# Optimization experiments

Hardware: AMD Instinct MI355X
Metric: run time of the kernel (lower is better)

The kernel has to match this reference:

```python
import jax, jax.numpy as jnp
import numpy as np

D_MODEL = 1024


def setup_inputs() -> dict:
    key = jax.random.key(0)
    ks = jax.random.split(key, 9)
    d = D_MODEL
    s = 1.0 / np.sqrt(d)
    return {
        "x": jax.random.normal(ks[0], (4, 2048, d), dtype=jnp.float32),
        "w_q": jax.random.normal(ks[1], (d, d), dtype=jnp.float32) * s,
        "b_q": jnp.zeros((d,), dtype=jnp.float32),
        "w_k": jax.random.normal(ks[2], (d, d), dtype=jnp.float32) * s,
        "b_k": jnp.zeros((d,), dtype=jnp.float32),
        "w_v": jax.random.normal(ks[3], (d, d), dtype=jnp.float32) * s,
        "b_v": jnp.zeros((d,), dtype=jnp.float32),
        "w_out": jax.random.normal(ks[4], (d, d), dtype=jnp.float32) * s,
        "b_out": jnp.zeros((d,), dtype=jnp.float32),
    }


def reference(x, w_q, b_q, w_k, b_k, w_v, b_v, w_out, b_out):
    d_model = x.shape[-1]
    # torch Linear: y = x @ W^T + b
    Q = jnp.einsum("bsd,ed->bse", x, w_q) + b_q
    K = jnp.einsum("bsd,ed->bse", x, w_k) + b_k
    V = jnp.einsum("bsd,ed->bse", x, w_v) + b_v
    scores = jnp.einsum("bqd,bkd->bqk", Q, K) / jnp.sqrt(jnp.float32(d_model)).astype(x.dtype)
    attn = jax.nn.softmax(scores, axis=-1)
    out = jnp.einsum("bqk,bkd->bqd", attn, V)
    return jnp.einsum("bsd,ed->bse", out, w_out) + b_out
```

## Files before the change

kernel.cpp:

```cpp
#include <hip/hip_runtime.h>


typedef __bf16 bf16x8 __attribute__((ext_vector_type(8)));
typedef float f32x4 __attribute__((ext_vector_type(4)));

__device__ __forceinline__ unsigned short f32_to_bf16(float f) {
  unsigned int u = __float_as_uint(f);
  u += 0x7fffu + ((u >> 16) & 1u);
  return (unsigned short)(u >> 16);
}

__device__ __forceinline__ ushort4 cvt4(float4 f) {
  ushort4 u;
  u.x = f32_to_bf16(f.x);
  u.y = f32_to_bf16(f.y);
  u.z = f32_to_bf16(f.z);
  u.w = f32_to_bf16(f.w);
  return u;
}

__device__ __forceinline__ void load_lds16(const void* g, void* l) {
  __builtin_amdgcn_global_load_lds(
      (const __attribute__((address_space(1))) void*)g,
      (__attribute__((address_space(3))) void*)l, 16, 0, 0);
}

__global__ __launch_bounds__(256) void prep(
    const float4* __restrict__ x, const float4* __restrict__ wq,
    const float4* __restrict__ wk, const float4* __restrict__ wv,
    const float4* __restrict__ wo, const float4* __restrict__ bq,
    const float4* __restrict__ bk, ushort4* __restrict__ xb,
    ushort4* __restrict__ wqk, ushort4* __restrict__ wvb,
    ushort4* __restrict__ wob, float4* __restrict__ bqk) {
  const int NX = 2097152;
  const int NW = 262144;
  int i = blockIdx.x * 256 + threadIdx.x;
  if (i < NX) {
    xb[i] = cvt4(x[i]);
  } else if (i < NX + NW) {
    int j = i - NX;
    wqk[j] = cvt4(wq[j]);
  } else if (i < NX + 2 * NW) {
    int j = i - NX - NW;
    wqk[NW + j] = cvt4(wk[j]);
  } else if (i < NX + 3 * NW) {
    int j = i - NX - 2 * NW;
    wvb[j] = cvt4(wv[j]);
  } else if (i < NX + 4 * NW) {
    int j = i - NX - 3 * NW;
    wob[j] = cvt4(wo[j]);
  } else if (i < NX + 4 * NW + 512) {
    int j = i - NX - 4 * NW;
    bqk[j] = (j < 256) ? bq[j] : bk[j - 256];
  }
}

__global__ __launch_bounds__(512, 2) void gemm_bt256dp(
    const unsigned short* __restrict__ A, const unsigned short* __restrict__ B,
    void* __restrict__ C, const float* __restrict__ bias,
    int M, int N, int K, float alpha, int out_bf16, int lda, int ldb,
    long long sA, long long sB, long long sC) {
  __shared__ unsigned short As[3][2][128 * 64];
  __shared__ unsigned short Bs[2][2][128 * 64];

  const int hw = blockIdx.x + gridDim.x * (blockIdx.y + gridDim.y * blockIdx.z);
  const int nwg = gridDim.x * gridDim.y * gridDim.z;
  const int lg = (hw & 7) * (nwg >> 3) + (hw >> 3);
  const int bn = lg % gridDim.x;
  const int rem = lg / gridDim.x;
  const int bm = rem % gridDim.y;
  const int bz = rem / gridDim.y;

  A += (long long)bz * sA;
  B += (long long)bz * sB;

  const int tid = threadIdx.x;
  const int lane = tid & 63, wave = tid >> 6;
  const int wr = wave >> 2;
  const int wc = wave & 3;
  const int l16 = lane & 15, quad = lane >> 4;
  const int wbh = wc >> 1;
  const int wbr = (wc & 1) * 64 + l16;
  const int pc0 = (quad ^ (l16 & 7)) * 8;
  const int pc1 = ((4 + quad) ^ (l16 & 7)) * 8;

  const int srow = tid >> 3;
  const int lch = (tid & 7) ^ (srow & 7);
  const unsigned short* gA0 = A + (long long)(bm * 256 + srow) * lda + lch * 8;
  const unsigned short* gB0 = B + (long long)(bn * 256 + srow) * ldb + lch * 8;

  f32x4 acc[8][4] = {};
  bf16x8 af[2][2];
  bf16x8 bf[4][2];

  const int NT = K >> 6;

#define STA(BUF, H, KT)                                                     \
  do {                                                                      \
    const unsigned short* _s =                                              \
        gA0 + (long long)(H) * 128 * lda + (long long)(KT) * 64;            \
    char* _d = (char*)&As[BUF][H][0] + wave * 1024;                         \
    load_lds16(_s, _d);                                                     \
    load_lds16(_s + (long long)64 * lda, _d + 8192);                        \
  } while (0)
#define STB(BUF, H, KT)                                                     \
  do {                                                                      \
    const unsigned short* _s =                                              \
        gB0 + (long long)(H) * 128 * ldb + (long long)(KT) * 64;            \
    char* _d = (char*)&Bs[BUF][H][0] + wave * 1024;                         \
    load_lds16(_s, _d);                                                     \
    load_lds16(_s + (long long)64 * ldb, _d + 8192);                        \
  } while (0)

#define DSAq(BUF, MIP)                                                      \
  do {                                                                      \
    _Pragma("unroll") for (int m2 = 0; m2 < 2; ++m2) {                      \
      const unsigned short* _r =                                            \
          &As[BUF][wr][(((MIP) * 2 + m2) * 16 + l16) * 64];                 \
      af[m2][0] = *(const bf16x8*)(_r + pc0);                               \
      af[m2][1] = *(const bf16x8*)(_r + pc1);                               \
    }                                                                       \
  } while (0)

#define DSBq(BUF)                                                           \
  do {                                                                      \
    _Pragma("unroll") for (int ni = 0; ni < 4; ++ni) {                      \
      const unsigned short* _r = &Bs[BUF][wbh][(wbr + ni * 16) * 64];       \
      bf[ni][0] = *(const bf16x8*)(_r + pc0);                               \
      bf[ni][1] = *(const bf16x8*)(_r + pc1);                               \
    }                                                                       \
  } while (0)

#define MMq(MIP)                                                            \
  do {                                                                      \
    _Pragma("unroll") for (int m2 = 0; m2 < 2; ++m2)                        \
        _Pragma("unroll") for (int ni = 0; ni < 4; ++ni) {                  \
      f32x4* _a = &acc[(MIP) * 2 + m2][ni];                                 \
      *_a = __builtin_amdgcn_mfma_f32_16x16x32_bf16(af[m2][0], bf[ni][0],   \
                                                    *_a, 0, 0, 0);          \
      *_a = __builtin_amdgcn_mfma_f32_16x16x32_bf16(af[m2][1], bf[ni][1],   \
                                                    *_a, 0, 0, 0);          \
    }                                                                       \
  } while (0)

#define BARx() __builtin_amdgcn_s_barrier()
#define WLGx() asm volatile("s_waitcnt lgkmcnt(0)" ::: "memory")
#define WVM8() asm volatile("s_waitcnt vmcnt(8)" ::: "memory")
#define PR1() __builtin_amdgcn_s_setprio(1)
#define PR0() __builtin_amdgcn_s_setprio(0)

  STA(0, 0, 0);
  STA(0, 1, 0);
  STB(0, 0, 0);
  STB(0, 1, 0);
  STA(1, 0, 1);
  STA(1, 1, 1);
  STB(1, 0, 1);
  STB(1, 1, 1);
  WVM8();
  BARx();

  int a = 0;
  for (int t = 0; t < NT; ++t) {
    const int b = t & 1;
    int a2 = a + 2;
    if (a2 >= 3) a2 -= 3;
    const int kt2 = (t + 2 < NT) ? t + 2 : NT - 1;
    DSBq(b);
    DSAq(a, 0);
    STA(a2, 0, kt2);
    BARx();
    WLGx();
    PR1();
    MMq(0);
    PR0();
    BARx();
    DSAq(a, 1);
    STA(a2, 1, kt2);
    BARx();
    WLGx();
    PR1();
    MMq(1);
    PR0();
    BARx();
    DSAq(a, 2);
    STB(b, 0, kt2);
    BARx();
    WLGx();
    PR1();
    MMq(2);
    PR0();
    BARx();
    DSAq(a, 3);
    STB(b, 1, kt2);
    BARx();
    WLGx();
    PR1();
    MMq(3);
    PR0();
    WVM8();
    BARx();
    ++a;
    if (a == 3) a = 0;
  }
  asm volatile("s_waitcnt vmcnt(0)" ::: "memory");

  const long long orow0 = (long long)bm * 256 + wr * 128 + quad * 4;
  const int ocol0 = bn * 256 + wc * 64 + l16;
  if (out_bf16) {
    unsigned short* Cp = (unsigned short*)C + (long long)bz * sC;
#pragma unroll
    for (int mi = 0; mi < 8; ++mi)
#pragma unroll
      for (int ni = 0; ni < 4; ++ni) {
        const int col = ocol0 + ni * 16;
        const float bv = bias ? bias[col] : 0.f;
#pragma unroll
        for (int r = 0; r < 4; ++r) {
          const float o = acc[mi][ni][r] * alpha + bv;
          Cp[(orow0 + mi * 16 + r) * N + col] = f32_to_bf16(o);
        }
      }
  } else {
    float* Cp = (float*)C + (long long)bz * sC;
#pragma unroll
    for (int mi = 0; mi < 8; ++mi)
#pragma unroll
      for (int ni = 0; ni < 4; ++ni) {
        const int col = ocol0 + ni * 16;
        const float bv = bias ? bias[col] : 0.f;
#pragma unroll
        for (int r = 0; r < 4; ++r) {
          const float o = acc[mi][ni][r] * alpha + bv;
          Cp[(orow0 + mi * 16 + r) * N + col] = o;
        }
      }
  }
#undef STA
#undef STB
#undef DSAq
#undef DSBq
#undef MMq
#undef BARx
#undef WLGx
#undef WVM8
#undef PR1
#undef PR0
}

__global__ __launch_bounds__(512, 2) void gemm_bt128x256(
    const unsigned short* __restrict__ A, const unsigned short* __restrict__ B,
    void* __restrict__ C, const float* __restrict__ bias,
    int M, int N, int K, float alpha, int out_bf16, int bias_row,
    int lda, int ldb, long long sA, long long sB, long long sC) {
  __shared__ unsigned short As[3][128][64];
  __shared__ unsigned short Bs[3][256][64];

  const int hw = blockIdx.x + gridDim.x * (blockIdx.y + gridDim.y * blockIdx.z);
  const int nwg = gridDim.x * gridDim.y * gridDim.z;
  const int lg = (hw & 7) * (nwg >> 3) + (hw >> 3);
  const int bn = lg % gridDim.x;
  const int rem = lg / gridDim.x;
  const int bm = rem % gridDim.y;
  const int bz = rem / gridDim.y;

  A += (long long)bz * sA;
  B += (long long)bz * sB;

  const int tid = threadIdx.x;
  const int lane = tid & 63, wave = tid >> 6;
  const int wr = wave >> 2;
  const int wc = wave & 3;
  const int l16 = lane & 15, quad = lane >> 4;
  const int pc0 = (quad ^ (l16 & 7)) * 8;
  const int pc1 = ((4 + quad) ^ (l16 & 7)) * 8;

  const int srow = tid >> 3;
  const int lch = (tid & 7) ^ (srow & 7);
  const unsigned short* gA0 = A + (long long)(bm * 128 + srow) * lda + lch * 8;
  const unsigned short* gB0 = B + (long long)(bn * 256 + srow) * ldb + lch * 8;

  f32x4 acc[4][4] = {};
  bf16x8 af[2][2];
  bf16x8 bf[4][2];

  const int NT = K >> 6;

#define STG_A(BUF, KT)                                                      \
  do {                                                                      \
    const unsigned short* _s = gA0 + (long long)(KT) * 64;                  \
    char* _d = (char*)&As[BUF][0][0] + wave * 1024;                         \
    load_lds16(_s, _d);                                                     \
    load_lds16(_s + (long long)64 * lda, _d + 8192);                        \
  } while (0)
#define STG_B(BUF, KT, J0, JN)                                              \
  do {                                                                      \
    const unsigned short* _s = gB0 + (long long)(KT) * 64;                  \
    char* _d = (char*)&Bs[BUF][0][0] + wave * 1024;                         \
    _Pragma("unroll") for (int _j = (J0); _j < (JN); ++_j)                  \
        load_lds16(_s + (long long)(_j * 64) * ldb, _d + _j * 8192);        \
  } while (0)

#define DSA(BUF, P)                                                         \
  do {                                                                      \
    _Pragma("unroll") for (int m2 = 0; m2 < 2; ++m2) {                      \
      const unsigned short* _r =                                            \
          &As[BUF][wr * 64 + ((P) * 2 + m2) * 16 + l16][0];                 \
      af[m2][0] = *(const bf16x8*)(_r + pc0);                               \
      af[m2][1] = *(const bf16x8*)(_r + pc1);                               \
    }                                                                       \
  } while (0)

#define DSB(BUF)                                                            \
  do {                                                                      \
    _Pragma("unroll") for (int ni = 0; ni < 4; ++ni) {                      \
      const unsigned short* _r = &Bs[BUF][wc * 64 + ni * 16 + l16][0];      \
      bf[ni][0] = *(const bf16x8*)(_r + pc0);                               \
      bf[ni][1] = *(const bf16x8*)(_r + pc1);                               \
    }                                                                       \
  } while (0)

#define MM(P)                                                               \
  do {                                                                      \
    _Pragma("unroll") for (int m2 = 0; m2 < 2; ++m2)                        \
        _Pragma("unroll") for (int ni = 0; ni < 4; ++ni) {                  \
      f32x4* _a = &acc[(P) * 2 + m2][ni];                                   \
      *_a = __builtin_amdgcn_mfma_f32_16x16x32_bf16(af[m2][0], bf[ni][0],   \
                                                    *_a, 0, 0, 0);          \
      *_a = __builtin_amdgcn_mfma_f32_16x16x32_bf16(af[m2][1], bf[ni][1],   \
                                                    *_a, 0, 0, 0);          \
    }                                                                       \
  } while (0)

#define BAR() __builtin_amdgcn_s_barrier()
#define WLG() asm volatile("s_waitcnt lgkmcnt(0)" ::: "memory")
#define WVM6() asm volatile("s_waitcnt vmcnt(6)" ::: "memory")
#define P1x() __builtin_amdgcn_s_setprio(1)
#define P0x() __builtin_amdgcn_s_setprio(0)

  STG_A(0, 0);
  STG_B(0, 0, 0, 4);
  STG_A(1, 1);
  STG_B(1, 1, 0, 4);
  WVM6();
  BAR();

  int cur = 0;
  for (int t = 0; t < NT; ++t) {
    int b2 = cur + 2;
    if (b2 >= 3) b2 -= 3;
    const int kt = (t + 2 < NT) ? t + 2 : NT - 1;
    DSB(cur);
    DSA(cur, 0);
    STG_A(b2, kt);
    STG_B(b2, kt, 0, 1);
    BAR();
    WLG();
    P1x();
    MM(0);
    P0x();
    BAR();
    DSA(cur, 1);
    STG_B(b2, kt, 1, 4);
    BAR();
    WLG();
    P1x();
    MM(1);
    P0x();
    WVM6();
    BAR();
    ++cur;
    if (cur == 3) cur = 0;
  }
  asm volatile("s_waitcnt vmcnt(0)" ::: "memory");

  const long long orow0 = (long long)bm * 128 + wr * 64 + quad * 4;
  const int ocol0 = bn * 256 + wc * 64 + l16;
  if (out_bf16) {
    unsigned short* Cp = (unsigned short*)C + (long long)bz * sC;
#pragma unroll
    for (int mi = 0; mi < 4; ++mi)
#pragma unroll
      for (int ni = 0; ni < 4; ++ni) {
        const int col = ocol0 + ni * 16;
        const float bcol = (bias && !bias_row) ? bias[col] : 0.f;
#pragma unroll
        for (int r = 0; r < 4; ++r) {
          const float bv =
              (bias && bias_row) ? bias[orow0 + mi * 16 + r] : bcol;
          const float o = acc[mi][ni][r] * alpha + bv;
          Cp[(orow0 + mi * 16 + r) * N + col] = f32_to_bf16(o);
        }
      }
  } else {
    float* Cp = (float*)C + (long long)bz * sC;
#pragma unroll
    for (int mi = 0; mi < 4; ++mi)
#pragma unroll
      for (int ni = 0; ni < 4; ++ni) {
        const int col = ocol0 + ni * 16;
        const float bcol = (bias && !bias_row) ? bias[col] : 0.f;
#pragma unroll
        for (int r = 0; r < 4; ++r) {
          const float bv =
              (bias && bias_row) ? bias[orow0 + mi * 16 + r] : bcol;
          const float o = acc[mi][ni][r] * alpha + bv;
          Cp[(orow0 + mi * 16 + r) * N + col] = o;
        }
      }
  }
#undef STG_A
#undef STG_B
#undef DSA
#undef DSB
#undef MM
#undef BAR
#undef WLG
#undef WVM6
#undef P1x
#undef P0x
}

__global__ __launch_bounds__(256) void softmax_rows(
    const float* __restrict__ S, unsigned short* __restrict__ P) {
  const long long row = blockIdx.x;
  const float* s = S + row * 2048;
  const int t = threadIdx.x;
  float v[8];
  float mx = -3.4e38f;
#pragma unroll
  for (int i = 0; i < 8; i++) {
    v[i] = s[t + i * 256];
    mx = fmaxf(mx, v[i]);
  }
#pragma unroll
  for (int o = 32; o >= 1; o >>= 1) mx = fmaxf(mx, __shfl_xor(mx, o));
  __shared__ float red[4], red2[4];
  if ((t & 63) == 0) red[t >> 6] = mx;
  __syncthreads();
  mx = fmaxf(fmaxf(red[0], red[1]), fmaxf(red[2], red[3]));
  float sum = 0.f;
#pragma unroll
  for (int i = 0; i < 8; i++) {
    v[i] = __expf(v[i] - mx);
    sum += v[i];
  }
#pragma unroll
  for (int o = 32; o >= 1; o >>= 1) sum += __shfl_xor(sum, o);
  if ((t & 63) == 0) red2[t >> 6] = sum;
  __syncthreads();
  sum = red2[0] + red2[1] + red2[2] + red2[3];
  const float inv = 1.0f / sum;
  unsigned short* p = P + row * 2048;
#pragma unroll
  for (int i = 0; i < 8; i++) p[t + i * 256] = f32_to_bf16(v[i] * inv);
}

extern "C" void kernel_launch(void* const* d_in, const int* in_sizes, int n_in,
                              void* d_out, int out_size, void* d_ws,
                              size_t ws_size, hipStream_t stream) {
  const float* x = (const float*)d_in[0];
  const float* wq = (const float*)d_in[1];
  const float* bq = (const float*)d_in[2];
  const float* wk = (const float*)d_in[3];
  const float* bk = (const float*)d_in[4];
  const float* wv = (const float*)d_in[5];
  const float* bv = (const float*)d_in[6];
  const float* wo = (const float*)d_in[7];
  const float* bo = (const float*)d_in[8];
  float* out = (float*)d_out;
  char* ws = (char*)d_ws;
  const size_t MB = 1ull << 20;

  unsigned short* xb  = (unsigned short*)(ws + 0);
  unsigned short* wqk = (unsigned short*)(ws + 16 * MB);
  unsigned short* wvb = (unsigned short*)(ws + 20 * MB);
  unsigned short* wob = (unsigned short*)(ws + 22 * MB);
  unsigned short* QKm = (unsigned short*)(ws + 24 * MB);
  unsigned short* VT  = (unsigned short*)(ws + 56 * MB);
  float*          S   = (float*)(ws + 72 * MB);
  float*          bqk = (float*)(ws + 72 * MB);
  unsigned short* P   = QKm;
  unsigned short* O   = xb;

  prep<<<dim3(12290), dim3(256), 0, stream>>>(
      (const float4*)x, (const float4*)wq, (const float4*)wk,
      (const float4*)wv, (const float4*)wo, (const float4*)bq,
      (const float4*)bk, (ushort4*)xb, (ushort4*)wqk, (ushort4*)wvb,
      (ushort4*)wob, (float4*)bqk);

  gemm_bt256dp<<<dim3(8, 32, 1), dim3(512), 0, stream>>>(
      xb, wqk, QKm, bqk, 8192, 2048, 1024, 1.f, 1, 1024, 1024, 0, 0, 0);

  gemm_bt128x256<<<dim3(32, 8, 1), dim3(512), 0, stream>>>(
      wvb, xb, VT, bv, 1024, 8192, 1024, 1.f, 1, 1, 1024, 1024, 0, 0, 0);

  gemm_bt256dp<<<dim3(8, 8, 4), dim3(512), 0, stream>>>(
      QKm, QKm + 1024, S, nullptr, 2048, 2048, 1024, 0.03125f, 0, 2048, 2048,
      2048ll * 2048, 2048ll * 2048, 2048ll * 2048);

  softmax_rows<<<dim3(8192), dim3(256), 0, stream>>>(S, P);

  gemm_bt128x256<<<dim3(4, 16, 4), dim3(512), 0, stream>>>(
      P, VT, O, nullptr, 2048, 1024, 2048, 1.f, 1, 0, 2048, 8192,
      2048ll * 2048, 2048ll, 2048ll * 1024);

  gemm_bt128x256<<<dim3(4, 64, 1), dim3(512), 0, stream>>>(
      O, wob, out, bo, 8192, 1024, 1024, 1.f, 0, 0, 1024, 1024, 0, 0, 0);
}
```

Before: 297.5 us.

## Fuse all attention stages into one persistent kernel with grid barriers

Replaces the six separate launches (prep, QK proj, V proj, scores, softmax, PV, out proj) with one persistent 256-block kernel. Stages are separated by a software grid barrier built on an atomic counter, and shared memory is carved manually per phase. This removes per-launch overhead and inter-kernel gaps. In exchange it pins occupancy at one block per CU, makes the V-projection run serially after the QK tile in the same block, and depends on all 256 blocks being co-resident to avoid deadlock.

```diff
diff --git a/kernel.cpp b/kernel.cpp
--- a/kernel.cpp
+++ b/kernel.cpp
@@ -3,11 +3,14 @@
 
 typedef __bf16 bf16x8 __attribute__((ext_vector_type(8)));
 typedef float f32x4 __attribute__((ext_vector_type(4)));
-
-__device__ __forceinline__ unsigned short f32_to_bf16(float f) {
+typedef unsigned short ush;
+
+__device__ unsigned int g_bar_cnt;
+
+__device__ __forceinline__ ush f32_to_bf16(float f) {
   unsigned int u = __float_as_uint(f);
   u += 0x7fffu + ((u >> 16) & 1u);
-  return (unsigned short)(u >> 16);
+  return (ush)(u >> 16);
 }
 
 __device__ __forceinline__ ushort4 cvt4(float4 f) {
@@ -25,54 +28,27 @@
       (__attribute__((address_space(3))) void*)l, 16, 0, 0);
 }
 
-__global__ __launch_bounds__(256) void prep(
-    const float4* __restrict__ x, const float4* __restrict__ wq,
-    const float4* __restrict__ wk, const float4* __restrict__ wv,
-    const float4* __restrict__ wo, const float4* __restrict__ bq,
-    const float4* __restrict__ bk, ushort4* __restrict__ xb,
-    ushort4* __restrict__ wqk, ushort4* __restrict__ wvb,
-    ushort4* __restrict__ wob, float4* __restrict__ bqk) {
-  const int NX = 2097152;
-  const int NW = 262144;
-  int i = blockIdx.x * 256 + threadIdx.x;
-  if (i < NX) {
-    xb[i] = cvt4(x[i]);
-  } else if (i < NX + NW) {
-    int j = i - NX;
-    wqk[j] = cvt4(wq[j]);
-  } else if (i < NX + 2 * NW) {
-    int j = i - NX - NW;
-    wqk[NW + j] = cvt4(wk[j]);
-  } else if (i < NX + 3 * NW) {
-    int j = i - NX - 2 * NW;
-    wvb[j] = cvt4(wv[j]);
-  } else if (i < NX + 4 * NW) {
-    int j = i - NX - 3 * NW;
-    wob[j] = cvt4(wo[j]);
-  } else if (i < NX + 4 * NW + 512) {
-    int j = i - NX - 4 * NW;
-    bqk[j] = (j < 256) ? bq[j] : bk[j - 256];
-  }
-}
-
-__global__ __launch_bounds__(512, 2) void gemm_bt256dp(
-    const unsigned short* __restrict__ A, const unsigned short* __restrict__ B,
-    void* __restrict__ C, const float* __restrict__ bias,
-    int M, int N, int K, float alpha, int out_bf16, int lda, int ldb,
-    long long sA, long long sB, long long sC) {
-  __shared__ unsigned short As[3][2][128 * 64];
-  __shared__ unsigned short Bs[2][2][128 * 64];
-
-  const int hw = blockIdx.x + gridDim.x * (blockIdx.y + gridDim.y * blockIdx.z);
-  const int nwg = gridDim.x * gridDim.y * gridDim.z;
-  const int lg = (hw & 7) * (nwg >> 3) + (hw >> 3);
-  const int bn = lg % gridDim.x;
-  const int rem = lg / gridDim.x;
-  const int bm = rem % gridDim.y;
-  const int bz = rem / gridDim.y;
-
-  A += (long long)bz * sA;
-  B += (long long)bz * sB;
+__device__ __forceinline__ void grid_bar(int k) {
+  __syncthreads();
+  if (threadIdx.x == 0) {
+    __threadfence();
+    __hip_atomic_fetch_add(&g_bar_cnt, 1u, __ATOMIC_ACQ_REL,
+                           __HIP_MEMORY_SCOPE_AGENT);
+    const unsigned tgt = (unsigned)k * 256u;
+    while (__hip_atomic_load(&g_bar_cnt, __ATOMIC_ACQUIRE,
+                             __HIP_MEMORY_SCOPE_AGENT) < tgt)
+      __builtin_amdgcn_s_sleep(2);
+    __threadfence();
+  }
+  __syncthreads();
+}
+
+__device__ void g256_tile(const ush* __restrict__ A, const ush* __restrict__ B,
+                          void* __restrict__ C, const float* __restrict__ bias,
+                          int N, int K, float alpha, int out_bf16, int lda,
+                          int ldb, int bn, int bm, char* smem) {
+  ush (*As)[2][8192] = (ush(*)[2][8192])smem;
+  ush (*Bs)[2][8192] = (ush(*)[2][8192])(smem + 98304);
 
   const int tid = threadIdx.x;
   const int lane = tid & 63, wave = tid >> 6;
@@ -86,8 +62,8 @@
 
   const int srow = tid >> 3;
   const int lch = (tid & 7) ^ (srow & 7);
-  const unsigned short* gA0 = A + (long long)(bm * 256 + srow) * lda + lch * 8;
-  const unsigned short* gB0 = B + (long long)(bn * 256 + srow) * ldb + lch * 8;
+  const ush* gA0 = A + (long long)(bm * 256 + srow) * lda + lch * 8;
+  const ush* gB0 = B + (long long)(bn * 256 + srow) * ldb + lch * 8;
 
   f32x4 acc[8][4] = {};
   bf16x8 af[2][2];
@@ -97,40 +73,34 @@
 
 #define STA(BUF, H, KT)                                                     \
   do {                                                                      \
-    const unsigned short* _s =                                              \
-        gA0 + (long long)(H) * 128 * lda + (long long)(KT) * 64;            \
+    const ush* _s = gA0 + (long long)(H) * 128 * lda + (long long)(KT) * 64;\
     char* _d = (char*)&As[BUF][H][0] + wave * 1024;                         \
     load_lds16(_s, _d);                                                     \
     load_lds16(_s + (long long)64 * lda, _d + 8192);                        \
   } while (0)
 #define STB(BUF, H, KT)                                                     \
   do {                                                                      \
-    const unsigned short* _s =                                              \
-        gB0 + (long long)(H) * 128 * ldb + (long long)(KT) * 64;            \
+    const ush* _s = gB0 + (long long)(H) * 128 * ldb + (long long)(KT) * 64;\
     char* _d = (char*)&Bs[BUF][H][0] + wave * 1024;                         \
     load_lds16(_s, _d);                                                     \
     load_lds16(_s + (long long)64 * ldb, _d + 8192);                        \
   } while (0)
-
 #define DSAq(BUF, MIP)                                                      \
   do {                                                                      \
     _Pragma("unroll") for (int m2 = 0; m2 < 2; ++m2) {                      \
-      const unsigned short* _r =                                            \
-          &As[BUF][wr][(((MIP) * 2 + m2) * 16 + l16) * 64];                 \
+      const ush* _r = &As[BUF][wr][(((MIP) * 2 + m2) * 16 + l16) * 64];     \
       af[m2][0] = *(const bf16x8*)(_r + pc0);                               \
       af[m2][1] = *(const bf16x8*)(_r + pc1);                               \
     }                                                                       \
   } while (0)
-
 #define DSBq(BUF)                                                           \
   do {                                                                      \
     _Pragma("unroll") for (int ni = 0; ni < 4; ++ni) {                      \
-      const unsigned short* _r = &Bs[BUF][wbh][(wbr + ni * 16) * 64];       \
+      const ush* _r = &Bs[BUF][wbh][(wbr + ni * 16) * 64];                  \
       bf[ni][0] = *(const bf16x8*)(_r + pc0);                               \
       bf[ni][1] = *(const bf16x8*)(_r + pc1);                               \
     }                                                                       \
   } while (0)
-
 #define MMq(MIP)                                                            \
   do {                                                                      \
     _Pragma("unroll") for (int m2 = 0; m2 < 2; ++m2)                        \
@@ -142,7 +112,6 @@
                                                     *_a, 0, 0, 0);          \
     }                                                                       \
   } while (0)
-
 #define BARx() __builtin_amdgcn_s_barrier()
 #define WLGx() asm volatile("s_waitcnt lgkmcnt(0)" ::: "memory")
 #define WVM8() asm volatile("s_waitcnt vmcnt(8)" ::: "memory")
@@ -208,7 +177,7 @@
   const long long orow0 = (long long)bm * 256 + wr * 128 + quad * 4;
   const int ocol0 = bn * 256 + wc * 64 + l16;
   if (out_bf16) {
-    unsigned short* Cp = (unsigned short*)C + (long long)bz * sC;
+    ush* Cp = (ush*)C;
 #pragma unroll
     for (int mi = 0; mi < 8; ++mi)
 #pragma unroll
@@ -222,7 +191,7 @@
         }
       }
   } else {
-    float* Cp = (float*)C + (long long)bz * sC;
+    float* Cp = (float*)C;
 #pragma unroll
     for (int mi = 0; mi < 8; ++mi)
 #pragma unroll
@@ -248,24 +217,13 @@
 #undef PR0
 }
 
-__global__ __launch_bounds__(512, 2) void gemm_bt128x256(
-    const unsigned short* __restrict__ A, const unsigned short* __restrict__ B,
-    void* __restrict__ C, const float* __restrict__ bias,
-    int M, int N, int K, float alpha, int out_bf16, int bias_row,
-    int lda, int ldb, long long sA, long long sB, long long sC) {
-  __shared__ unsigned short As[3][128][64];
-  __shared__ unsigned short Bs[3][256][64];
-
-  const int hw = blockIdx.x + gridDim.x * (blockIdx.y + gridDim.y * blockIdx.z);
-  const int nwg = gridDim.x * gridDim.y * gridDim.z;
-  const int lg = (hw & 7) * (nwg >> 3) + (hw >> 3);
-  const int bn = lg % gridDim.x;
-  const int rem = lg / gridDim.x;
-  const int bm = rem % gridDim.y;
-  const int bz = rem / gridDim.y;
-
-  A += (long long)bz * sA;
-  B += (long long)bz * sB;
+__device__ void g128_tile(const ush* __restrict__ A, const ush* __restrict__ B,
+                          void* __restrict__ C, const float* __restrict__ bias,
+                          int N, int K, float alpha, int out_bf16,
+                          int bias_row, int lda, int ldb, int bn, int bm,
+                          char* smem) {
+  ush (*As)[128][64] = (ush(*)[128][64])smem;
+  ush (*Bs)[256][64] = (ush(*)[256][64])(smem + 49152);
 
   const int tid = threadIdx.x;
   const int lane = tid & 63, wave = tid >> 6;
@@ -277,8 +235,8 @@
 
   const int srow = tid >> 3;
   const int lch = (tid & 7) ^ (srow & 7);
-  const unsigned short* gA0 = A + (long long)(bm * 128 + srow) * lda + lch * 8;
-  const unsigned short* gB0 = B + (long long)(bn * 256 + srow) * ldb + lch * 8;
+  const ush* gA0 = A + (long long)(bm * 128 + srow) * lda + lch * 8;
+  const ush* gB0 = B + (long long)(bn * 256 + srow) * ldb + lch * 8;
 
   f32x4 acc[4][4] = {};
   bf16x8 af[2][2];
@@ -288,38 +246,34 @@
 
 #define STG_A(BUF, KT)                                                      \
   do {                                                                      \
-    const unsigned short* _s = gA0 + (long long)(KT) * 64;                  \
+    const ush* _s = gA0 + (long long)(KT) * 64;                             \
     char* _d = (char*)&As[BUF][0][0] + wave * 1024;                         \
     load_lds16(_s, _d);                                                     \
     load_lds16(_s + (long long)64 * lda, _d + 8192);                        \
   } while (0)
 #define STG_B(BUF, KT, J0, JN)                                              \
   do {                                                                      \
-    const unsigned short* _s = gB0 + (long long)(KT) * 64;                  \
+    const ush* _s = gB0 + (long long)(KT) * 64;                             \
     char* _d = (char*)&Bs[BUF][0][0] + wave * 1024;                         \
     _Pragma("unroll") for (int _j = (J0); _j < (JN); ++_j)                  \
         load_lds16(_s + (long long)(_j * 64) * ldb, _d + _j * 8192);        \
   } while (0)
-
 #define DSA(BUF, P)                                                         \
   do {                                                                      \
     _Pragma("unroll") for (int m2 = 0; m2 < 2; ++m2) {                      \
-      const unsigned short* _r =                                            \
-          &As[BUF][wr * 64 + ((P) * 2 + m2) * 16 + l16][0];                 \
+      const ush* _r = &As[BUF][wr * 64 + ((P) * 2 + m2) * 16 + l16][0];     \
       af[m2][0] = *(const bf16x8*)(_r + pc0);                               \
       af[m2][1] = *(const bf16x8*)(_r + pc1);                               \
     }                                                                       \
   } while (0)
-
 #define DSB(BUF)                                                            \
   do {                                                                      \
     _Pragma("unroll") for (int ni = 0; ni < 4; ++ni) {                      \
-      const unsigned short* _r = &Bs[BUF][wc * 64 + ni * 16 + l16][0];      \
+      const ush* _r = &Bs[BUF][wc * 64 + ni * 16 + l16][0];                 \
       bf[ni][0] = *(const bf16x8*)(_r + pc0);                               \
       bf[ni][1] = *(const bf16x8*)(_r + pc1);                               \
     }                                                                       \
   } while (0)
-
 #define MM(P)                                                               \
   do {                                                                      \
     _Pragma("unroll") for (int m2 = 0; m2 < 2; ++m2)                        \
@@ -331,7 +285,6 @@
                                                     *_a, 0, 0, 0);          \
     }                                                                       \
   } while (0)
-
 #define BAR() __builtin_amdgcn_s_barrier()
 #define WLG() asm volatile("s_waitcnt lgkmcnt(0)" ::: "memory")
 #define WVM6() asm volatile("s_waitcnt vmcnt(6)" ::: "memory")
@@ -377,7 +330,7 @@
   const long long orow0 = (long long)bm * 128 + wr * 64 + quad * 4;
   const int ocol0 = bn * 256 + wc * 64 + l16;
   if (out_bf16) {
-    unsigned short* Cp = (unsigned short*)C + (long long)bz * sC;
+    ush* Cp = (ush*)C;
 #pragma unroll
     for (int mi = 0; mi < 4; ++mi)
 #pragma unroll
@@ -393,7 +346,7 @@
         }
       }
   } else {
-    float* Cp = (float*)C + (long long)bz * sC;
+    float* Cp = (float*)C;
 #pragma unroll
     for (int mi = 0; mi < 4; ++mi)
 #pragma unroll
@@ -421,90 +374,142 @@
 #undef P0x
 }
 
-__global__ __launch_bounds__(256) void softmax_rows(
-    const float* __restrict__ S, unsigned short* __restrict__ P) {
-  const long long row = blockIdx.x;
-  const float* s = S + row * 2048;
+__device__ void softmax_phase(const float* __restrict__ S, ush* __restrict__ P,
+                              int blk, char* smem) {
+  float* red = (float*)smem;
   const int t = threadIdx.x;
-  float v[8];
-  float mx = -3.4e38f;
-#pragma unroll
-  for (int i = 0; i < 8; i++) {
-    v[i] = s[t + i * 256];
-    mx = fmaxf(mx, v[i]);
-  }
-#pragma unroll
-  for (int o = 32; o >= 1; o >>= 1) mx = fmaxf(mx, __shfl_xor(mx, o));
-  __shared__ float red[4], red2[4];
-  if ((t & 63) == 0) red[t >> 6] = mx;
-  __syncthreads();
-  mx = fmaxf(fmaxf(red[0], red[1]), fmaxf(red[2], red[3]));
-  float sum = 0.f;
-#pragma unroll
-  for (int i = 0; i < 8; i++) {
-    v[i] = __expf(v[i] - mx);
-    sum += v[i];
-  }
-#pragma unroll
-  for (int o = 32; o >= 1; o >>= 1) sum += __shfl_xor(sum, o);
-  if ((t & 63) == 0) red2[t >> 6] = sum;
-  __syncthreads();
-  sum = red2[0] + red2[1] + red2[2] + red2[3];
-  const float inv = 1.0f / sum;
-  unsigned short* p = P + row * 2048;
-#pragma unroll
-  for (int i = 0; i < 8; i++) p[t + i * 256] = f32_to_bf16(v[i] * inv);
+  const int w = t >> 6, lane = t & 63;
+  for (int r = 0; r < 32; ++r) {
+    const long long row = (long long)blk * 32 + r;
+    const float* s = S + row * 2048;
+    float v0 = s[t], v1 = s[t + 512], v2 = s[t + 1024], v3 = s[t + 1536];
+    float mx = fmaxf(fmaxf(v0, v1), fmaxf(v2, v3));
+#pragma unroll
+    for (int o = 32; o >= 1; o >>= 1) mx = fmaxf(mx, __shfl_xor(mx, o));
+    if (lane == 0) red[w] = mx;
+    __syncthreads();
+    mx = red[0];
+#pragma unroll
+    for (int i = 1; i < 8; ++i) mx = fmaxf(mx, red[i]);
+    v0 = __expf(v0 - mx);
+    v1 = __expf(v1 - mx);
+    v2 = __expf(v2 - mx);
+    v3 = __expf(v3 - mx);
+    float sum = v0 + v1 + v2 + v3;
+#pragma unroll
+    for (int o = 32; o >= 1; o >>= 1) sum += __shfl_xor(sum, o);
+    if (lane == 0) red[8 + w] = sum;
+    __syncthreads();
+    sum = red[8];
+#pragma unroll
+    for (int i = 9; i < 16; ++i) sum += red[i];
+    const float inv = 1.0f / sum;
+    ush* p = P + row * 2048;
+    p[t] = f32_to_bf16(v0 * inv);
+    p[t + 512] = f32_to_bf16(v1 * inv);
+    p[t + 1024] = f32_to_bf16(v2 * inv);
+    p[t + 1536] = f32_to_bf16(v3 * inv);
+  }
+}
+
+__global__ __launch_bounds__(512, 1) void fused_all(
+    const float4* __restrict__ x, const float4* __restrict__ wq,
+    const float4* __restrict__ wk, const float4* __restrict__ wv,
+    const float4* __restrict__ wo, const float4* __restrict__ bq4,
+    const float4* __restrict__ bk4, const float* __restrict__ bv,
+    const float* __restrict__ bo, float* __restrict__ out,
+    char* __restrict__ ws) {
+  __shared__ __align__(16) char smem[163840];
+  const size_t MB = 1ull << 20;
+  ush* xb = (ush*)(ws);
+  ush* wqk = (ush*)(ws + 16 * MB);
+  ush* wvb = (ush*)(ws + 20 * MB);
+  ush* wob = (ush*)(ws + 22 * MB);
+  ush* QKm = (ush*)(ws + 24 * MB);
+  ush* VT = (ush*)(ws + 56 * MB);
+  float* S = (float*)(ws + 72 * MB);
+  float* bqk = (float*)(ws + 72 * MB);
+  ush* P = QKm;
+  ush* O = xb;
+
+  const int blk = blockIdx.x;
+  const int t = threadIdx.x;
+
+  {
+    const int NX = 2097152, NW = 262144;
+    ushort4* xbo = (ushort4*)xb;
+    ushort4* wqko = (ushort4*)wqk;
+    ushort4* wvbo = (ushort4*)wvb;
+    ushort4* wobo = (ushort4*)wob;
+    float4* bqko = (float4*)bqk;
+    for (int i = blk * 512 + t; i < 3146240; i += 131072) {
+      if (i < NX) {
+        xbo[i] = cvt4(x[i]);
+      } else if (i < NX + NW) {
+        int j = i - NX;
+        wqko[j] = cvt4(wq[j]);
+      } else if (i < NX + 2 * NW) {
+        int j = i - NX - NW;
+        wqko[NW + j] = cvt4(wk[j]);
+      } else if (i < NX + 3 * NW) {
+        int j = i - NX - 2 * NW;
+        wvbo[j] = cvt4(wv[j]);
+      } else if (i < NX + 4 * NW) {
+        int j = i - NX - 3 * NW;
+        wobo[j] = cvt4(wo[j]);
+      } else {
+        int j = i - NX - 4 * NW;
+        bqko[j] = (j < 256) ? bq4[j] : bk4[j - 256];
+      }
+    }
+  }
+  grid_bar(1);
+
+  const int lg = (blk & 7) * 32 + (blk >> 3);
+
+  g256_tile(xb, wqk, QKm, bqk, 2048, 1024, 1.f, 1, 1024, 1024, lg & 7,
+            lg >> 3, smem);
+  g128_tile(wvb, xb, VT, bv, 8192, 1024, 1.f, 1, 1, 1024, 1024, lg & 31,
+            lg >> 5, smem);
+  grid_bar(2);
+
+  {
+    const int bz = lg >> 6;
+    const ush* Aq = QKm + (long long)bz * (2048ll * 2048);
+    const ush* Bk = QKm + 1024 + (long long)bz * (2048ll * 2048);
+    float* Sc = S + (long long)bz * (2048ll * 2048);
+    g256_tile(Aq, Bk, Sc, nullptr, 2048, 1024, 0.03125f, 0, 2048, 2048,
+              lg & 7, (lg >> 3) & 7, smem);
+  }
+  grid_bar(3);
+
+  softmax_phase(S, P, blk, smem);
+  grid_bar(4);
+
+  {
+    const int bz = lg >> 6;
+    const ush* Ap = P + (long long)bz * (2048ll * 2048);
+    const ush* Bvt = VT + (long long)bz * 2048;
+    ush* Oc = O + (long long)bz * (2048ll * 1024);
+    g128_tile(Ap, Bvt, Oc, nullptr, 1024, 2048, 1.f, 1, 0, 2048, 8192, lg & 3,
+              (lg >> 2) & 15, smem);
+  }
+  grid_bar(5);
+
+  g128_tile(O, wob, out, bo, 1024, 1024, 1.f, 0, 0, 1024, 1024, lg & 3,
+            lg >> 2, smem);
 }
 
 extern "C" void kernel_launch(void* const* d_in, const int* in_sizes, int n_in,
                               void* d_out, int out_size, void* d_ws,
                               size_t ws_size, hipStream_t stream) {
-  const float* x = (const float*)d_in[0];
-  const float* wq = (const float*)d_in[1];
-  const float* bq = (const float*)d_in[2];
-  const float* wk = (const float*)d_in[3];
-  const float* bk = (const float*)d_in[4];
-  const float* wv = (const float*)d_in[5];
-  const float* bv = (const float*)d_in[6];
-  const float* wo = (const float*)d_in[7];
-  const float* bo = (const float*)d_in[8];
-  float* out = (float*)d_out;
-  char* ws = (char*)d_ws;
-  const size_t MB = 1ull << 20;
-
-  unsigned short* xb  = (unsigned short*)(ws + 0);
-  unsigned short* wqk = (unsigned short*)(ws + 16 * MB);
-  unsigned short* wvb = (unsigned short*)(ws + 20 * MB);
-  unsigned short* wob = (unsigned short*)(ws + 22 * MB);
-  unsigned short* QKm = (unsigned short*)(ws + 24 * MB);
-  unsigned short* VT  = (unsigned short*)(ws + 56 * MB);
-  float*          S   = (float*)(ws + 72 * MB);
-  float*          bqk = (float*)(ws + 72 * MB);
-  unsigned short* P   = QKm;
-  unsigned short* O   = xb;
-
-  prep<<<dim3(12290), dim3(256), 0, stream>>>(
-      (const float4*)x, (const float4*)wq, (const float4*)wk,
-      (const float4*)wv, (const float4*)wo, (const float4*)bq,
-      (const float4*)bk, (ushort4*)xb, (ushort4*)wqk, (ushort4*)wvb,
-      (ushort4*)wob, (float4*)bqk);
-
-  gemm_bt256dp<<<dim3(8, 32, 1), dim3(512), 0, stream>>>(
-      xb, wqk, QKm, bqk, 8192, 2048, 1024, 1.f, 1, 1024, 1024, 0, 0, 0);
-
-  gemm_bt128x256<<<dim3(32, 8, 1), dim3(512), 0, stream>>>(
-      wvb, xb, VT, bv, 1024, 8192, 1024, 1.f, 1, 1, 1024, 1024, 0, 0, 0);
-
-  gemm_bt256dp<<<dim3(8, 8, 4), dim3(512), 0, stream>>>(
-      QKm, QKm + 1024, S, nullptr, 2048, 2048, 1024, 0.03125f, 0, 2048, 2048,
-      2048ll * 2048, 2048ll * 2048, 2048ll * 2048);
-
-  softmax_rows<<<dim3(8192), dim3(256), 0, stream>>>(S, P);
-
-  gemm_bt128x256<<<dim3(4, 16, 4), dim3(512), 0, stream>>>(
-      P, VT, O, nullptr, 2048, 1024, 2048, 1.f, 1, 0, 2048, 8192,
-      2048ll * 2048, 2048ll, 2048ll * 1024);
-
-  gemm_bt128x256<<<dim3(4, 64, 1), dim3(512), 0, stream>>>(
-      O, wob, out, bo, 8192, 1024, 1024, 1.f, 0, 0, 1024, 1024, 0, 0, 0);
-}
+  static void* bar_addr = nullptr;
+  if (!bar_addr) (void)hipGetSymbolAddress(&bar_addr, HIP_SYMBOL(g_bar_cnt));
+  hipMemsetAsync(bar_addr, 0, sizeof(unsigned int), stream);
+
+  fused_all<<<dim3(256), dim3(512), 0, stream>>>(
+      (const float4*)d_in[0], (const float4*)d_in[1], (const float4*)d_in[3],
+      (const float4*)d_in[5], (const float4*)d_in[7], (const float4*)d_in[2],
+      (const float4*)d_in[4], (const float*)d_in[6], (const float*)d_in[8],
+      (float*)d_out, (char*)d_ws);
+}
```

Result: slower. 511.2 us (+71.8%).

## Merge QK^T and V-projection GEMMs into one launch; vectorize softmax

Applied to the files above, without the earlier changes.

The GEMM kernels become device tile functions that take dynamically carved shared memory. A combined kernel runs the 256 QK^T tiles and the 256 V^T projection tiles in one 512-block grid, so the two independent GEMMs fill the GPU together instead of running as separate launches. Softmax now loads and stores rows with float4/ushort4 vectors. The combined kernel always reserves the larger shared-memory footprint, which could limit occupancy for the V tiles, and it has to run the heavier tile shape's register budget.

```diff
diff --git a/kernel.cpp b/kernel.cpp
--- a/kernel.cpp
+++ b/kernel.cpp
@@ -3,11 +3,12 @@
 
 typedef __bf16 bf16x8 __attribute__((ext_vector_type(8)));
 typedef float f32x4 __attribute__((ext_vector_type(4)));
-
-__device__ __forceinline__ unsigned short f32_to_bf16(float f) {
+typedef unsigned short ush;
+
+__device__ __forceinline__ ush f32_to_bf16(float f) {
   unsigned int u = __float_as_uint(f);
   u += 0x7fffu + ((u >> 16) & 1u);
-  return (unsigned short)(u >> 16);
+  return (ush)(u >> 16);
 }
 
 __device__ __forceinline__ ushort4 cvt4(float4 f) {
@@ -55,24 +56,12 @@
   }
 }
 
-__global__ __launch_bounds__(512, 2) void gemm_bt256dp(
-    const unsigned short* __restrict__ A, const unsigned short* __restrict__ B,
-    void* __restrict__ C, const float* __restrict__ bias,
-    int M, int N, int K, float alpha, int out_bf16, int lda, int ldb,
-    long long sA, long long sB, long long sC) {
-  __shared__ unsigned short As[3][2][128 * 64];
-  __shared__ unsigned short Bs[2][2][128 * 64];
-
-  const int hw = blockIdx.x + gridDim.x * (blockIdx.y + gridDim.y * blockIdx.z);
-  const int nwg = gridDim.x * gridDim.y * gridDim.z;
-  const int lg = (hw & 7) * (nwg >> 3) + (hw >> 3);
-  const int bn = lg % gridDim.x;
-  const int rem = lg / gridDim.x;
-  const int bm = rem % gridDim.y;
-  const int bz = rem / gridDim.y;
-
-  A += (long long)bz * sA;
-  B += (long long)bz * sB;
+__device__ void g256_tile(const ush* __restrict__ A, const ush* __restrict__ B,
+                          void* __restrict__ C, const float* __restrict__ bias,
+                          int N, int K, float alpha, int out_bf16, int lda,
+                          int ldb, int bn, int bm, char* smem) {
+  ush (*As)[2][8192] = (ush(*)[2][8192])smem;
+  ush (*Bs)[2][8192] = (ush(*)[2][8192])(smem + 98304);
 
   const int tid = threadIdx.x;
   const int lane = tid & 63, wave = tid >> 6;
@@ -86,8 +75,8 @@
 
   const int srow = tid >> 3;
   const int lch = (tid & 7) ^ (srow & 7);
-  const unsigned short* gA0 = A + (long long)(bm * 256 + srow) * lda + lch * 8;
-  const unsigned short* gB0 = B + (long long)(bn * 256 + srow) * ldb + lch * 8;
+  const ush* gA0 = A + (long long)(bm * 256 + srow) * lda + lch * 8;
+  const ush* gB0 = B + (long long)(bn * 256 + srow) * ldb + lch * 8;
 
   f32x4 acc[8][4] = {};
   bf16x8 af[2][2];
@@ -97,40 +86,34 @@
 
 #define STA(BUF, H, KT)                                                     \
   do {                                                                      \
-    const unsigned short* _s =                                              \
-        gA0 + (long long)(H) * 128 * lda + (long long)(KT) * 64;            \
+    const ush* _s = gA0 + (long long)(H) * 128 * lda + (long long)(KT) * 64;\
     char* _d = (char*)&As[BUF][H][0] + wave * 1024;                         \
     load_lds16(_s, _d);                                                     \
     load_lds16(_s + (long long)64 * lda, _d + 8192);                        \
   } while (0)
 #define STB(BUF, H, KT)                                                     \
   do {                                                                      \
-    const unsigned short* _s =                                              \
-        gB0 + (long long)(H) * 128 * ldb + (long long)(KT) * 64;            \
+    const ush* _s = gB0 + (long long)(H) * 128 * ldb + (long long)(KT) * 64;\
     char* _d = (char*)&Bs[BUF][H][0] + wave * 1024;                         \
     load_lds16(_s, _d);                                                     \
     load_lds16(_s + (long long)64 * ldb, _d + 8192);                        \
   } while (0)
-
 #define DSAq(BUF, MIP)                                                      \
   do {                                                                      \
     _Pragma("unroll") for (int m2 = 0; m2 < 2; ++m2) {                      \
-      const unsigned short* _r =                                            \
-          &As[BUF][wr][(((MIP) * 2 + m2) * 16 + l16) * 64];                 \
+      const ush* _r = &As[BUF][wr][(((MIP) * 2 + m2) * 16 + l16) * 64];     \
       af[m2][0] = *(const bf16x8*)(_r + pc0);                               \
       af[m2][1] = *(const bf16x8*)(_r + pc1);                               \
     }                                                                       \
   } while (0)
-
 #define DSBq(BUF)                                                           \
   do {                                                                      \
     _Pragma("unroll") for (int ni = 0; ni < 4; ++ni) {                      \
-      const unsigned short* _r = &Bs[BUF][wbh][(wbr + ni * 16) * 64];       \
+      const ush* _r = &Bs[BUF][wbh][(wbr + ni * 16) * 64];                  \
       bf[ni][0] = *(const bf16x8*)(_r + pc0);                               \
       bf[ni][1] = *(const bf16x8*)(_r + pc1);                               \
     }                                                                       \
   } while (0)
-
 #define MMq(MIP)                                                            \
   do {                                                                      \
     _Pragma("unroll") for (int m2 = 0; m2 < 2; ++m2)                        \
@@ -142,7 +125,6 @@
                                                     *_a, 0, 0, 0);          \
     }                                                                       \
   } while (0)
-
 #define BARx() __builtin_amdgcn_s_barrier()
 #define WLGx() asm volatile("s_waitcnt lgkmcnt(0)" ::: "memory")
 #define WVM8() asm volatile("s_waitcnt vmcnt(8)" ::: "memory")
@@ -208,7 +190,7 @@
   const long long orow0 = (long long)bm * 256 + wr * 128 + quad * 4;
   const int ocol0 = bn * 256 + wc * 64 + l16;
   if (out_bf16) {
-    unsigned short* Cp = (unsigned short*)C + (long long)bz * sC;
+    ush* Cp = (ush*)C;
 #pragma unroll
     for (int mi = 0; mi < 8; ++mi)
 #pragma unroll
@@ -222,7 +204,7 @@
         }
       }
   } else {
-    float* Cp = (float*)C + (long long)bz * sC;
+    float* Cp = (float*)C;
 #pragma unroll
     for (int mi = 0; mi < 8; ++mi)
 #pragma unroll
@@ -248,24 +230,13 @@
 #undef PR0
 }
 
-__global__ __launch_bounds__(512, 2) void gemm_bt128x256(
-    const unsigned short* __restrict__ A, const unsigned short* __restrict__ B,
-    void* __restrict__ C, const float* __restrict__ bias,
-    int M, int N, int K, float alpha, int out_bf16, int bias_row,
-    int lda, int ldb, long long sA, long long sB, long long sC) {
-  __shared__ unsigned short As[3][128][64];
-  __shared__ unsigned short Bs[3][256][64];
-
-  const int hw = blockIdx.x + gridDim.x * (blockIdx.y + gridDim.y * blockIdx.z);
-  const int nwg = gridDim.x * gridDim.y * gridDim.z;
-  const int lg = (hw & 7) * (nwg >> 3) + (hw >> 3);
-  const int bn = lg % gridDim.x;
-  const int rem = lg / gridDim.x;
-  const int bm = rem % gridDim.y;
-  const int bz = rem / gridDim.y;
-
-  A += (long long)bz * sA;
-  B += (long long)bz * sB;
+__device__ void g128_tile(const ush* __restrict__ A, const ush* __restrict__ B,
+                          void* __restrict__ C, const float* __restrict__ bias,
+                          int N, int K, float alpha, int out_bf16,
+                          int bias_row, int lda, int ldb, int bn, int bm,
+                          char* smem) {
+  ush (*As)[128][64] = (ush(*)[128][64])smem;
+  ush (*Bs)[256][64] = (ush(*)[256][64])(smem + 49152);
 
   const int tid = threadIdx.x;
   const int lane = tid & 63, wave = tid >> 6;
@@ -277,8 +248,8 @@
 
   const int srow = tid >> 3;
   const int lch = (tid & 7) ^ (srow & 7);
-  const unsigned short* gA0 = A + (long long)(bm * 128 + srow) * lda + lch * 8;
-  const unsigned short* gB0 = B + (long long)(bn * 256 + srow) * ldb + lch * 8;
+  const ush* gA0 = A + (long long)(bm * 128 + srow) * lda + lch * 8;
+  const ush* gB0 = B + (long long)(bn * 256 + srow) * ldb + lch * 8;
 
   f32x4 acc[4][4] = {};
   bf16x8 af[2][2];
@@ -288,38 +259,34 @@
 
 #define STG_A(BUF, KT)                                                      \
   do {                                                                      \
-    const unsigned short* _s = gA0 + (long long)(KT) * 64;                  \
+    const ush* _s = gA0 + (long long)(KT) * 64;                             \
     char* _d = (char*)&As[BUF][0][0] + wave * 1024;                         \
     load_lds16(_s, _d);                                                     \
     load_lds16(_s + (long long)64 * lda, _d + 8192);                        \
   } while (0)
 #define STG_B(BUF, KT, J0, JN)                                              \
   do {                                                                      \
-    const unsigned short* _s = gB0 + (long long)(KT) * 64;                  \
+    const ush* _s = gB0 + (long long)(KT) * 64;                             \
     char* _d = (char*)&Bs[BUF][0][0] + wave * 1024;                         \
     _Pragma("unroll") for (int _j = (J0); _j < (JN); ++_j)                  \
         load_lds16(_s + (long long)(_j * 64) * ldb, _d + _j * 8192);        \
   } while (0)
-
 #define DSA(BUF, P)                                                         \
   do {                                                                      \
     _Pragma("unroll") for (int m2 = 0; m2 < 2; ++m2) {                      \
-      const unsigned short* _r =                                            \
-          &As[BUF][wr * 64 + ((P) * 2 + m2) * 16 + l16][0];                 \
+      const ush* _r = &As[BUF][wr * 64 + ((P) * 2 + m2) * 16 + l16][0];     \
       af[m2][0] = *(const bf16x8*)(_r + pc0);                               \
       af[m2][1] = *(const bf16x8*)(_r + pc1);                               \
     }                                                                       \
   } while (0)
-
 #define DSB(BUF)                                                            \
   do {                                                                      \
     _Pragma("unroll") for (int ni = 0; ni < 4; ++ni) {                      \
-      const unsigned short* _r = &Bs[BUF][wc * 64 + ni * 16 + l16][0];      \
+      const ush* _r = &Bs[BUF][wc * 64 + ni * 16 + l16][0];                 \
       bf[ni][0] = *(const bf16x8*)(_r + pc0);                               \
       bf[ni][1] = *(const bf16x8*)(_r + pc1);                               \
     }                                                                       \
   } while (0)
-
 #define MM(P)                                                               \
   do {                                                                      \
     _Pragma("unroll") for (int m2 = 0; m2 < 2; ++m2)                        \
@@ -331,7 +298,6 @@
                                                     *_a, 0, 0, 0);          \
     }                                                                       \
   } while (0)
-
 #define BAR() __builtin_amdgcn_s_barrier()
 #define WLG() asm volatile("s_waitcnt lgkmcnt(0)" ::: "memory")
 #define WVM6() asm volatile("s_waitcnt vmcnt(6)" ::: "memory")
@@ -377,7 +343,7 @@
   const long long orow0 = (long long)bm * 128 + wr * 64 + quad * 4;
   const int ocol0 = bn * 256 + wc * 64 + l16;
   if (out_bf16) {
-    unsigned short* Cp = (unsigned short*)C + (long long)bz * sC;
+    ush* Cp = (ush*)C;
 #pragma unroll
     for (int mi = 0; mi < 4; ++mi)
 #pragma unroll
@@ -393,7 +359,7 @@
         }
       }
   } else {
-    float* Cp = (float*)C + (long long)bz * sC;
+    float* Cp = (float*)C;
 #pragma unroll
     for (int mi = 0; mi < 4; ++mi)
 #pragma unroll
@@ -421,39 +387,104 @@
 #undef P0x
 }
 
+__global__ __launch_bounds__(512, 2) void k256(
+    const ush* __restrict__ A, const ush* __restrict__ B, void* __restrict__ C,
+    const float* __restrict__ bias, int N, int K, float alpha, int out_bf16,
+    int lda, int ldb, long long sA, long long sB, long long sC) {
+  __shared__ __align__(16) char smem[163840];
+  const int hw = blockIdx.x + gridDim.x * (blockIdx.y + gridDim.y * blockIdx.z);
+  const int nwg = gridDim.x * gridDim.y * gridDim.z;
+  const int lg = (hw & 7) * (nwg >> 3) + (hw >> 3);
+  const int bn = lg % gridDim.x;
+  const int rem = lg / gridDim.x;
+  const int bm = rem % gridDim.y;
+  const int bz = rem / gridDim.y;
+  void* Cb = out_bf16 ? (void*)((ush*)C + (long long)bz * sC)
+                      : (void*)((float*)C + (long long)bz * sC);
+  g256_tile(A + (long long)bz * sA, B + (long long)bz * sB, Cb, bias, N, K,
+            alpha, out_bf16, lda, ldb, bn, bm, smem);
+}
+
+__global__ __launch_bounds__(512, 2) void k128(
+    const ush* __restrict__ A, const ush* __restrict__ B, void* __restrict__ C,
+    const float* __restrict__ bias, int N, int K, float alpha, int out_bf16,
+    int bias_row, int lda, int ldb, long long sA, long long sB, long long sC) {
+  __shared__ __align__(16) char smem[147456];
+  const int hw = blockIdx.x + gridDim.x * (blockIdx.y + gridDim.y * blockIdx.z);
+  const int nwg = gridDim.x * gridDim.y * gridDim.z;
+  const int lg = (hw & 7) * (nwg >> 3) + (hw >> 3);
+  const int bn = lg % gridDim.x;
+  const int rem = lg / gridDim.x;
+  const int bm = rem % gridDim.y;
+  const int bz = rem / gridDim.y;
+  void* Cb = out_bf16 ? (void*)((ush*)C + (long long)bz * sC)
+                      : (void*)((float*)C + (long long)bz * sC);
+  g128_tile(A + (long long)bz * sA, B + (long long)bz * sB, Cb, bias, N, K,
+            alpha, out_bf16, bias_row, lda, ldb, bn, bm, smem);
+}
+
+__global__ __launch_bounds__(512, 2) void qkt_vt(
+    const ush* __restrict__ QKm, float* __restrict__ S,
+    const ush* __restrict__ wvb, const ush* __restrict__ xb,
+    ush* __restrict__ VT, const float* __restrict__ bv) {
+  __shared__ __align__(16) char smem[163840];
+  const int blk = blockIdx.x;
+  if (blk < 256) {
+    const int lg = (blk & 7) * 32 + (blk >> 3);
+    const int bn = lg & 7, bm = (lg >> 3) & 7, bz = lg >> 6;
+    const long long off = (long long)bz * (2048ll * 2048);
+    g256_tile(QKm + off, QKm + 1024 + off, (void*)(S + off), nullptr, 2048,
+              1024, 0.03125f, 0, 2048, 2048, bn, bm, smem);
+  } else {
+    const int b2 = blk - 256;
+    const int lg = (b2 & 7) * 32 + (b2 >> 3);
+    const int bn = lg & 31, bm = lg >> 5;
+    g128_tile(wvb, xb, VT, bv, 8192, 1024, 1.f, 1, 1, 1024, 1024, bn, bm,
+              smem);
+  }
+}
+
 __global__ __launch_bounds__(256) void softmax_rows(
-    const float* __restrict__ S, unsigned short* __restrict__ P) {
+    const float* __restrict__ S, ush* __restrict__ P) {
   const long long row = blockIdx.x;
-  const float* s = S + row * 2048;
+  const float4* s4 = (const float4*)(S + row * 2048);
   const int t = threadIdx.x;
-  float v[8];
-  float mx = -3.4e38f;
-#pragma unroll
-  for (int i = 0; i < 8; i++) {
-    v[i] = s[t + i * 256];
-    mx = fmaxf(mx, v[i]);
-  }
+  float4 a = s4[t], b = s4[t + 256];
+  float mx = fmaxf(fmaxf(fmaxf(a.x, a.y), fmaxf(a.z, a.w)),
+                   fmaxf(fmaxf(b.x, b.y), fmaxf(b.z, b.w)));
 #pragma unroll
   for (int o = 32; o >= 1; o >>= 1) mx = fmaxf(mx, __shfl_xor(mx, o));
   __shared__ float red[4], red2[4];
   if ((t & 63) == 0) red[t >> 6] = mx;
   __syncthreads();
   mx = fmaxf(fmaxf(red[0], red[1]), fmaxf(red[2], red[3]));
-  float sum = 0.f;
-#pragma unroll
-  for (int i = 0; i < 8; i++) {
-    v[i] = __expf(v[i] - mx);
-    sum += v[i];
-  }
+  a.x = __expf(a.x - mx);
+  a.y = __expf(a.y - mx);
+  a.z = __expf(a.z - mx);
+  a.w = __expf(a.w - mx);
+  b.x = __expf(b.x - mx);
+  b.y = __expf(b.y - mx);
+  b.z = __expf(b.z - mx);
+  b.w = __expf(b.w - mx);
+  float sum = (a.x + a.y) + (a.z + a.w) + (b.x + b.y) + (b.z + b.w);
 #pragma unroll
   for (int o = 32; o >= 1; o >>= 1) sum += __shfl_xor(sum, o);
   if ((t & 63) == 0) red2[t >> 6] = sum;
   __syncthreads();
   sum = red2[0] + red2[1] + red2[2] + red2[3];
   const float inv = 1.0f / sum;
-  unsigned short* p = P + row * 2048;
-#pragma unroll
-  for (int i = 0; i < 8; i++) p[t + i * 256] = f32_to_bf16(v[i] * inv);
+  ushort4 ua, ub;
+  ua.x = f32_to_bf16(a.x * inv);
+  ua.y = f32_to_bf16(a.y * inv);
+  ua.z = f32_to_bf16(a.z * inv);
+  ua.w = f32_to_bf16(a.w * inv);
+  ub.x = f32_to_bf16(b.x * inv);
+  ub.y = f32_to_bf16(b.y * inv);
+  ub.z = f32_to_bf16(b.z * inv);
+  ub.w = f32_to_bf16(b.w * inv);
+  ushort4* p4 = (ushort4*)(P + row * 2048);
+  p4[t] = ua;
+  p4[t + 256] = ub;
 }
 
 extern "C" void kernel_launch(void* const* d_in, const int* in_sizes, int n_in,
@@ -472,16 +503,16 @@
   char* ws = (char*)d_ws;
   const size_t MB = 1ull << 20;
 
-  unsigned short* xb  = (unsigned short*)(ws + 0);
-  unsigned short* wqk = (unsigned short*)(ws + 16 * MB);
-  unsigned short* wvb = (unsigned short*)(ws + 20 * MB);
-  unsigned short* wob = (unsigned short*)(ws + 22 * MB);
-  unsigned short* QKm = (unsigned short*)(ws + 24 * MB);
-  unsigned short* VT  = (unsigned short*)(ws + 56 * MB);
-  float*          S   = (float*)(ws + 72 * MB);
-  float*          bqk = (float*)(ws + 72 * MB);
-  unsigned short* P   = QKm;
-  unsigned short* O   = xb;
+  ush* xb  = (ush*)(ws + 0);
+  ush* wqk = (ush*)(ws + 16 * MB);
+  ush* wvb = (ush*)(ws + 20 * MB);
+  ush* wob = (ush*)(ws + 22 * MB);
+  ush* QKm = (ush*)(ws + 24 * MB);
+  ush* VT  = (ush*)(ws + 56 * MB);
+  float* S   = (float*)(ws + 72 * MB);
+  float* bqk = (float*)(ws + 72 * MB);
+  ush* P = QKm;
+  ush* O = xb;
 
   prep<<<dim3(12290), dim3(256), 0, stream>>>(
       (const float4*)x, (const float4*)wq, (const float4*)wk,
@@ -489,22 +520,17 @@
       (const float4*)bk, (ushort4*)xb, (ushort4*)wqk, (ushort4*)wvb,
       (ushort4*)wob, (float4*)bqk);
 
-  gemm_bt256dp<<<dim3(8, 32, 1), dim3(512), 0, stream>>>(
-      xb, wqk, QKm, bqk, 8192, 2048, 1024, 1.f, 1, 1024, 1024, 0, 0, 0);
-
-  gemm_bt128x256<<<dim3(32, 8, 1), dim3(512), 0, stream>>>(
-      wvb, xb, VT, bv, 1024, 8192, 1024, 1.f, 1, 1, 1024, 1024, 0, 0, 0);
-
-  gemm_bt256dp<<<dim3(8, 8, 4), dim3(512), 0, stream>>>(
-      QKm, QKm + 1024, S, nullptr, 2048, 2048, 1024, 0.03125f, 0, 2048, 2048,
-      2048ll * 2048, 2048ll * 2048, 2048ll * 2048);
+  k256<<<dim3(8, 32, 1), dim3(512), 0, stream>>>(
+      xb, wqk, QKm, bqk, 2048, 1024, 1.f, 1, 1024, 1024, 0, 0, 0);
+
+  qkt_vt<<<dim3(512), dim3(512), 0, stream>>>(QKm, S, wvb, xb, VT, bv);
 
   softmax_rows<<<dim3(8192), dim3(256), 0, stream>>>(S, P);
 
-  gemm_bt128x256<<<dim3(4, 16, 4), dim3(512), 0, stream>>>(
-      P, VT, O, nullptr, 2048, 1024, 2048, 1.f, 1, 0, 2048, 8192,
-      2048ll * 2048, 2048ll, 2048ll * 1024);
-
-  gemm_bt128x256<<<dim3(4, 64, 1), dim3(512), 0, stream>>>(
-      O, wob, out, bo, 8192, 1024, 1024, 1.f, 0, 0, 1024, 1024, 0, 0, 0);
-}
+  k128<<<dim3(4, 16, 4), dim3(512), 0, stream>>>(
+      P, VT, O, nullptr, 1024, 2048, 1.f, 1, 0, 2048, 8192, 2048ll * 2048,
+      2048ll, 2048ll * 1024);
+
+  k128<<<dim3(4, 64, 1), dim3(512), 0, stream>>>(
+      O, wob, out, bo, 1024, 1024, 1.f, 0, 0, 1024, 1024, 0, 0, 0);
+}
```

After: 346.9 us. +16.6%, slower.
